# Kernel tuning notes

Measured on AMD Instinct MI355X. Metric: run time of the kernel, lower is better.

Reference implementation:

```python
import jax, jax.numpy as jnp
import numpy as np
import math

N, D, H, E = 4096, 128, 8, 131072
HD = D // H  # head_dim = 16
SCALE = 1.0 / math.sqrt(HD)


def ln(x, g, b, eps=1e-5):
    m = x.mean(-1, keepdims=True)
    v = ((x - m) ** 2).mean(-1, keepdims=True)
    return (x - m) * jax.lax.rsqrt(v + eps) * g + b


def setup_inputs() -> dict:
    key = jax.random.key(0)
    ks = iter(jax.random.split(key, 40))

    def lin(out_d, in_d):
        w = jax.random.normal(next(ks), (out_d, in_d), jnp.float32) / math.sqrt(in_d)
        b = jnp.zeros((out_d,), jnp.float32)
        return w, b

    x = jax.random.normal(next(ks), (N, D), jnp.float32)
    edge_index = jax.random.randint(next(ks), (2, E), 0, N, dtype=jnp.int64)
    wq_l, bq_l = lin(D, D); wk_l, bk_l = lin(D, D); wv_l, bv_l = lin(D, D)
    wg, bg = lin(D, 2 * D)
    wq_g, bq_g = lin(D, D); wk_g, bk_g = lin(D, D); wv_g, bv_g = lin(D, D)
    wo_g, bo_g = lin(D, D)
    wf, bf = lin(D, 2 * D)
    gf = jnp.ones((D,), jnp.float32); betaf = jnp.zeros((D,), jnp.float32)
    w1, b1 = lin(4 * D, D); w2, b2 = lin(D, 4 * D)
    g1 = jnp.ones((D,), jnp.float32); be1 = jnp.zeros((D,), jnp.float32)
    g2 = jnp.ones((D,), jnp.float32); be2 = jnp.zeros((D,), jnp.float32)
    return dict(x=x, edge_index=edge_index,
                wq_l=wq_l, bq_l=bq_l, wk_l=wk_l, bk_l=bk_l, wv_l=wv_l, bv_l=bv_l,
                wg=wg, bg=bg,
                wq_g=wq_g, bq_g=bq_g, wk_g=wk_g, bk_g=bk_g, wv_g=wv_g, bv_g=bv_g,
                wo_g=wo_g, bo_g=bo_g,
                wf=wf, bf=bf, gf=gf, betaf=betaf,
                w1=w1, b1=b1, w2=w2, b2=b2,
                g1=g1, be1=be1, g2=g2, be2=be2)


def reference(x, edge_index, wq_l, bq_l, wk_l, bk_l, wv_l, bv_l, wg, bg,
              wq_g, bq_g, wk_g, bk_g, wv_g, bv_g, wo_g, bo_g,
              wf, bf, gf, betaf, w1, b1, w2, b2, g1, be1, g2, be2):
    src, dst = edge_index[0], edge_index[1]  # PyG: j=source, i=target
    # ---- local edge-indexed multi-head attention (GraphInteractionModule) ----
    Q = (x @ wq_l.T + bq_l).reshape(N, H, HD)
    K = (x @ wk_l.T + bk_l).reshape(N, H, HD)
    V = (x @ wv_l.T + bv_l).reshape(N, H, HD)
    attn = (Q[dst] * K[src]).sum(-1) * SCALE            # [E, H]
    m = jax.ops.segment_max(attn, dst, num_segments=N)  # [N, H]
    e = jnp.exp(attn - m[dst])
    s = jax.ops.segment_sum(e, dst, num_segments=N)
    alpha = e / s[dst]                                  # segment softmax over edges into each dst
    agg = jax.ops.segment_sum(V[src] * alpha[..., None], dst, num_segments=N).reshape(N, D)
    gate = jax.nn.sigmoid(jnp.concatenate([x, agg], axis=-1) @ wg.T + bg)
    local = gate * agg + (1.0 - gate) * x
    # ---- global dense MHA over all nodes (B=1) ----
    xn = ln(x, g1, be1)
    q = (xn @ wq_g.T + bq_g).reshape(N, H, HD)
    k = (xn @ wk_g.T + bk_g).reshape(N, H, HD)
    v = (xn @ wv_g.T + bv_g).reshape(N, H, HD)
    scores = jnp.einsum('nhd,mhd->hnm', q, k) * SCALE   # [H, N, N]
    p = jax.nn.softmax(scores, axis=-1)
    go = jnp.einsum('hnm,mhd->nhd', p, v).reshape(N, D) @ wo_g.T + bo_g
    # ---- fusion + residual + FFN ----
    fused = jax.nn.relu(ln(jnp.concatenate([local, go], axis=-1) @ wf.T + bf, gf, betaf))
    h = x + fused
    h2 = ln(h, g2, be2)
    out = h + (jax.nn.gelu(h2 @ w1.T + b1, approximate=False) @ w2.T + b2)
    return out
```

## Files before the change

### kernel.cpp

```cpp
#include <hip/hip_runtime.h>
#include <math.h>

#define NN 4096
#define DM 128
#define NE 131072
#define BCAP 96
#define QSCALE 0.36067376022224085f
#define ESCALE 0.36067376022224085f

typedef short short8 __attribute__((ext_vector_type(8)));
typedef float f32x4  __attribute__((ext_vector_type(4)));
typedef unsigned int uint4v __attribute__((ext_vector_type(4)));

static __device__ __forceinline__ unsigned pk2(float lo, float hi) {
  union { float f; unsigned u; } a, b; a.f = lo; b.f = hi;
  return __builtin_amdgcn_perm(b.u + 0x8000u, a.u + 0x8000u, 0x07060302u);
}
static __device__ __forceinline__ unsigned pkp(float lo, float hi) {
  union { float f; unsigned u; } a, b; a.f = lo; b.f = hi;
  return __builtin_amdgcn_perm(b.u, a.u, 0x07060302u);
}
static __device__ __forceinline__ unsigned short f2bh(float f) {
  union { float f; unsigned u; } v; v.f = f;
  return (unsigned short)((v.u + 0x8000u) >> 16);
}
static __device__ __forceinline__ float b2f16(unsigned short u) {
  union { unsigned u; float f; } v; v.u = ((unsigned)u) << 16; return v.f;
}
static __device__ __forceinline__ float blo(unsigned u) {
  union { unsigned u; float f; } v; v.u = u << 16; return v.f;
}
static __device__ __forceinline__ float bhi(unsigned u) {
  union { unsigned u; float f; } v; v.u = u & 0xffff0000u; return v.f;
}
static __device__ __forceinline__ short8 cvt8(float4 a, float4 b) {
  uint4v u;
  u.x = pk2(a.x, a.y); u.y = pk2(a.z, a.w);
  u.z = pk2(b.x, b.y); u.w = pk2(b.z, b.w);
  return __builtin_bit_cast(short8, u);
}
static __device__ __forceinline__ int detect64(const int* __restrict__ EI) {
  int v = EI[2 * (threadIdx.x & 63) + 1];
  for (int off = 1; off < 64; off <<= 1) v |= __shfl_xor(v, off);
  return (v == 0) ? 1 : 0;
}

__global__ __launch_bounds__(256) void k_fill(float* __restrict__ out, float v, int n) {
  int i = blockIdx.x * 256 + threadIdx.x;
  if (i < n) out[i] = v;
}

#define LN1(V, GV, BV) V = (V - mean) * rstd * GV + BV
__global__ __launch_bounds__(256) void gemm_six(
    const float* __restrict__ X,
    const float* __restrict__ G1, const float* __restrict__ Be1,
    const float* __restrict__ W0, const float* __restrict__ W1, const float* __restrict__ W2,
    const float* __restrict__ W3, const float* __restrict__ W4, const float* __restrict__ W5,
    const float* __restrict__ B0, const float* __restrict__ B1, const float* __restrict__ B2,
    const float* __restrict__ B3, const float* __restrict__ B4, const float* __restrict__ B5,
    void* __restrict__ O0, void* __restrict__ O1, void* __restrict__ O2,
    void* __restrict__ O3, void* __restrict__ O4, void* __restrict__ O5,
    int* __restrict__ deg,
    const float* __restrict__ WFp, const float* __restrict__ WOg, const float* __restrict__ BOg,
    float* __restrict__ WCp, float* __restrict__ BFp)
{
  __shared__ short Asm[2][64][40];
  __shared__ short Wsm[2][64][40];
  if (blockIdx.y == 12) {
    if (blockIdx.x >= 16) return;
    const int c = threadIdx.x & 127;
    const int f0 = blockIdx.x * 8 + (threadIdx.x >> 7) * 4;
    const float* wf0 = WFp + (size_t)(f0 + 0) * 256 + 128;
    const float* wf1 = WFp + (size_t)(f0 + 1) * 256 + 128;
    const float* wf2 = WFp + (size_t)(f0 + 2) * 256 + 128;
    const float* wf3 = WFp + (size_t)(f0 + 3) * 256 + 128;
    float a0v = 0.f, a1v = 0.f, a2v = 0.f, a3v = 0.f;
    float c0 = 0.f, c1 = 0.f, c2 = 0.f, c3 = 0.f;
#pragma unroll 4
    for (int n = 0; n < 128; n++) {
      float wo = WOg[(size_t)n * 128 + c];
      float bv = BOg[n];
      float w0 = wf0[n], w1 = wf1[n], w2 = wf2[n], w3 = wf3[n];
      a0v += w0 * wo; a1v += w1 * wo; a2v += w2 * wo; a3v += w3 * wo;
      c0 += w0 * bv; c1 += w1 * bv; c2 += w2 * bv; c3 += w3 * bv;
    }
    WCp[(size_t)(f0 + 0) * 128 + c] = a0v;
    WCp[(size_t)(f0 + 1) * 128 + c] = a1v;
    WCp[(size_t)(f0 + 2) * 128 + c] = a2v;
    WCp[(size_t)(f0 + 3) * 128 + c] = a3v;
    if (c == 0) { BFp[f0] = c0; BFp[f0 + 1] = c1; BFp[f0 + 2] = c2; BFp[f0 + 3] = c3; }
    return;
  }
  if (blockIdx.x == 0 && blockIdx.y == 0) {
#pragma unroll
    for (int i = 0; i < 16; i++) deg[threadIdx.x * 16 + i] = 0;
  }
  const int g = blockIdx.y >> 1;
  const float* Wt  = (g==0)?W0:(g==1)?W1:(g==2)?W2:(g==3)?W3:(g==4)?W4:W5;
  const float* Bia = (g==0)?B0:(g==1)?B1:(g==2)?B2:(g==3)?B3:(g==4)?B4:B5;
  void* Cp         = (g==0)?O0:(g==1)?O1:(g==2)?O2:(g==3)?O3:(g==4)?O4:O5;
  const int omode  = (g==4)?3:(g==5)?2:1;
  const float osc  = (g==3)? QSCALE : (g==0)? ESCALE : 1.f;
  const int m0 = blockIdx.x * 64, n0 = (blockIdx.y & 1) * 64;
  const int tid = threadIdx.x;
  const int srow = tid >> 2, koff = (tid & 3) * 8;
  const int lane = tid & 63, wave = tid >> 6;
  const int quad = lane >> 4, m16 = lane & 15;

  const float* arow = X + (size_t)(m0 + srow) * 128 + koff;
  float4 a0[4], a1[4];
#pragma unroll
  for (int c = 0; c < 4; c++) {
    a0[c] = *(const float4*)(arow + c * 32);
    a1[c] = *(const float4*)(arow + c * 32 + 4);
  }
  if (g >= 3) {
    float s = 0.f;
#pragma unroll
    for (int c = 0; c < 4; c++)
      s += a0[c].x + a0[c].y + a0[c].z + a0[c].w + a1[c].x + a1[c].y + a1[c].z + a1[c].w;
    s += __shfl_xor(s, 1); s += __shfl_xor(s, 2);
    float mean = s * (1.0f / 128.0f);
    float v = 0.f;
#pragma unroll
    for (int c = 0; c < 4; c++) {
      float d;
      d = a0[c].x - mean; v += d*d;  d = a0[c].y - mean; v += d*d;
      d = a0[c].z - mean; v += d*d;  d = a0[c].w - mean; v += d*d;
      d = a1[c].x - mean; v += d*d;  d = a1[c].y - mean; v += d*d;
      d = a1[c].z - mean; v += d*d;  d = a1[c].w - mean; v += d*d;
    }
    v += __shfl_xor(v, 1); v += __shfl_xor(v, 2);
    float rstd = rsqrtf(v * (1.0f / 128.0f) + 1e-5f);
#pragma unroll
    for (int c = 0; c < 4; c++) {
      const int col = c * 32 + koff;
      float4 gv0 = *(const float4*)(G1 + col),  gv1 = *(const float4*)(G1 + col + 4);
      float4 bv0 = *(const float4*)(Be1 + col), bv1 = *(const float4*)(Be1 + col + 4);
      LN1(a0[c].x, gv0.x, bv0.x); LN1(a0[c].y, gv0.y, bv0.y);
      LN1(a0[c].z, gv0.z, bv0.z); LN1(a0[c].w, gv0.w, bv0.w);
      LN1(a1[c].x, gv1.x, bv1.x); LN1(a1[c].y, gv1.y, bv1.y);
      LN1(a1[c].z, gv1.z, bv1.z); LN1(a1[c].w, gv1.w, bv1.w);
    }
  }

  f32x4 acc[4];
#pragma unroll
  for (int i = 0; i < 4; i++) acc[i] = {0.f, 0.f, 0.f, 0.f};
  float4 w0r, w1r;
  {
    const float* wp = Wt + (size_t)(n0 + srow) * 128 + koff;
    w0r = *(const float4*)wp; w1r = *(const float4*)(wp + 4);
  }
#pragma unroll
  for (int c = 0; c < 4; c++) {
    const int cur = c & 1;
    *(short8*)&Asm[cur][srow][koff] = cvt8(a0[c], a1[c]);
    *(short8*)&Wsm[cur][srow][koff] = cvt8(w0r, w1r);
    __syncthreads();
    if (c < 3) {
      const float* wp = Wt + (size_t)(n0 + srow) * 128 + (c + 1) * 32 + koff;
      w0r = *(const float4*)wp; w1r = *(const float4*)(wp + 4);
    }
    short8 af = *(short8*)&Asm[cur][wave * 16 + m16][quad * 8];
#pragma unroll
    for (int nt = 0; nt < 4; nt++) {
      short8 bf = *(short8*)&Wsm[cur][nt * 16 + m16][quad * 8];
      acc[nt] = __builtin_amdgcn_mfma_f32_16x16x32_bf16(af, bf, acc[nt], 0, 0, 0);
    }
  }
#pragma unroll
  for (int nt = 0; nt < 4; nt++) {
#pragma unroll
    for (int r = 0; r < 4; r++) {
      const int m = m0 + wave * 16 + quad * 4 + r;
      const int n = n0 + nt * 16 + m16;
      float v = (acc[nt][r] + Bia[n]) * osc;
      size_t oi = (size_t)m * 128 + n;
      if (omode == 1)      ((unsigned short*)Cp)[oi] = f2bh(v);
      else if (omode == 3) ((unsigned short*)Cp)[(size_t)(n >> 4) * (NN * 16) + (size_t)m * 16 + (n & 15)] = f2bh(v);
      else                 ((unsigned short*)Cp)[(size_t)n * NN + m] = f2bh(v);
    }
  }
}

__global__ __launch_bounds__(512) void k_attn_fused(
    const unsigned short* __restrict__ Kh, const unsigned short* __restrict__ Qb,
    const unsigned short* __restrict__ VT, float* __restrict__ O,
    const int* __restrict__ EI, int* __restrict__ deg, int* __restrict__ EL)
{
  __shared__ float LO[8][4][16][16];
  __shared__ float LL[8][4][16];
  if (blockIdx.x >= 512) {
    int is64 = detect64(EI);
    int base = (blockIdx.x - 512) * 2048 + threadIdx.x;
#pragma unroll
    for (int r = 0; r < 4; r++) {
      int e = base + r * 512;
      int d = is64 ? EI[2*(NE+e)] : EI[NE+e];
      d = min(max(d, 0), NN-1);
      int slot = atomicAdd(&deg[d], 1);
      if (slot < BCAP) EL[d * BCAP + slot] = e;
    }
    return;
  }
  const int h = blockIdx.x >> 6, qt = blockIdx.x & 63;
  const int tid = threadIdx.x, lane = tid & 63, wave = tid >> 6;
  const int quad = lane >> 4, m16 = lane & 15;
  const int r0 = qt * 64;
  const short8 z8 = {0,0,0,0,0,0,0,0};
  const f32x4  z4 = {0.f,0.f,0.f,0.f};
  short8 qf[4] = {z8, z8, z8, z8};
  if (quad < 2) {
#pragma unroll
    for (int j = 0; j < 4; j++)
      qf[j] = *(const short8*)(Qb + (size_t)(r0 + j * 16 + m16) * DM + h * 16 + quad * 8);
  }
  short8 ones;
#pragma unroll
  for (int i = 0; i < 8; i++) ones[i] = (short)0x3F80;
  const int kperm = (m16 >> 2) * 8 + (m16 & 3);
  const int kbase = wave * 512;
  const unsigned short* khead = Kh + (size_t)h * (NN * 16);
  f32x4 acc[4] = {z4, z4, z4, z4};
  f32x4 acc2[4] = {z4, z4, z4, z4};
  short8 a0 = z8, a1 = z8, a2 = z8, a3 = z8;
  for (int kt = 0; kt < 8; kt++) {
    const int key0 = kbase + kt * 64;
    if (quad < 2) {
      const unsigned short* kp = khead + (size_t)(key0 + kperm) * 16 + quad * 8;
      a0 = *(const short8*)kp;
      a1 = *(const short8*)(kp + 4 * 16);
      a2 = *(const short8*)(kp + 32 * 16);
      a3 = *(const short8*)(kp + 36 * 16);
    }
    const unsigned short* vp = VT + (size_t)(h * 16 + m16) * NN + key0 + quad * 8;
    short8 av0 = *(const short8*)vp;
    short8 av1 = *(const short8*)(vp + 32);
#pragma unroll
    for (int j = 0; j < 4; j++) {
      f32x4 s0 = __builtin_amdgcn_mfma_f32_16x16x32_bf16(a0, qf[j], z4, 0, 0, 0);
      f32x4 s1 = __builtin_amdgcn_mfma_f32_16x16x32_bf16(a1, qf[j], z4, 0, 0, 0);
      f32x4 s2 = __builtin_amdgcn_mfma_f32_16x16x32_bf16(a2, qf[j], z4, 0, 0, 0);
      f32x4 s3 = __builtin_amdgcn_mfma_f32_16x16x32_bf16(a3, qf[j], z4, 0, 0, 0);
      float e0 = __builtin_amdgcn_exp2f(s0[0]), e1 = __builtin_amdgcn_exp2f(s0[1]);
      float e2 = __builtin_amdgcn_exp2f(s0[2]), e3 = __builtin_amdgcn_exp2f(s0[3]);
      float e4 = __builtin_amdgcn_exp2f(s1[0]), e5 = __builtin_amdgcn_exp2f(s1[1]);
      float e6 = __builtin_amdgcn_exp2f(s1[2]), e7 = __builtin_amdgcn_exp2f(s1[3]);
      uint4v u;
      u.x = pkp(e0, e1); u.y = pkp(e2, e3); u.z = pkp(e4, e5); u.w = pkp(e6, e7);
      short8 p0 = __builtin_bit_cast(short8, u);
      float f0 = __builtin_amdgcn_exp2f(s2[0]), f1 = __builtin_amdgcn_exp2f(s2[1]);
      float f2 = __builtin_amdgcn_exp2f(s2[2]), f3 = __builtin_amdgcn_exp2f(s2[3]);
      float f4 = __builtin_amdgcn_exp2f(s3[0]), f5 = __builtin_amdgcn_exp2f(s3[1]);
      float f6 = __builtin_amdgcn_exp2f(s3[2]), f7 = __builtin_amdgcn_exp2f(s3[3]);
      uint4v w;
      w.x = pkp(f0, f1); w.y = pkp(f2, f3); w.z = pkp(f4, f5); w.w = pkp(f6, f7);
      short8 p1 = __builtin_bit_cast(short8, w);
      acc[j]  = __builtin_amdgcn_mfma_f32_16x16x32_bf16(av0, p0, acc[j], 0, 0, 0);
      acc[j]  = __builtin_amdgcn_mfma_f32_16x16x32_bf16(av1, p1, acc[j], 0, 0, 0);
      acc2[j] = __builtin_amdgcn_mfma_f32_16x16x32_bf16(ones, p0, acc2[j], 0, 0, 0);
      acc2[j] = __builtin_amdgcn_mfma_f32_16x16x32_bf16(ones, p1, acc2[j], 0, 0, 0);
    }
  }
#pragma unroll
  for (int j = 0; j < 4; j++) {
    float4 a4; a4.x = acc[j][0]; a4.y = acc[j][1]; a4.z = acc[j][2]; a4.w = acc[j][3];
    *(float4*)&LO[wave][j][m16][quad * 4] = a4;
    if (lane < 16) LL[wave][j][lane] = acc2[j][0];
  }
  __syncthreads();
  if (wave < 4) {
    const int j = wave;
    float4 o = *(float4*)&LO[0][j][m16][quad * 4];
    float lt = LL[0][j][m16];
#pragma unroll
    for (int w2 = 1; w2 < 8; w2++) {
      float4 t = *(float4*)&LO[w2][j][m16][quad * 4];
      o.x += t.x; o.y += t.y; o.z += t.z; o.w += t.w;
      lt += LL[w2][j][m16];
    }
    float inv = 1.0f / fmaxf(lt, 1e-30f);
    float4 r4; r4.x = o.x * inv; r4.y = o.y * inv; r4.z = o.z * inv; r4.w = o.w * inv;
    *(float4*)(O + (size_t)(r0 + j * 16 + m16) * DM + h * 16 + quad * 4) = r4;
  }
}

__global__ __launch_bounds__(256) void k_edge_agg3(const int* __restrict__ EI,
    const int* __restrict__ deg, const int* __restrict__ elist,
    const unsigned short* __restrict__ Vl, const unsigned short* __restrict__ Kb,
    const unsigned short* __restrict__ Qb, float* __restrict__ AG) {
  __shared__ float PS[2][128];
  __shared__ float SSH[2][2][8];
  __shared__ float SC[2][BCAP][8];
  int is64 = detect64(EI);
  int tid = threadIdx.x;
  int dsti = tid >> 7;
  int half = (tid >> 6) & 1;
  int lane = tid & 63;
  int d = blockIdx.x * 2 + dsti;
  int degd = min(deg[d], BCAP), start = d * BCAP;
  int hh = lane >> 3;
  unsigned qv = *(const unsigned*)(Qb + (size_t)d * DM + 2 * lane);
  float q0 = blo(qv), q1 = bhi(qv);
  float ss = 0.f;
  int i = half;
  for (; i + 6 < degd; i += 8) {
    int e0 = elist[start+i], e1 = elist[start+i+2], e2 = elist[start+i+4], e3 = elist[start+i+6];
    e0 = min(max(e0,0),NE-1); e1 = min(max(e1,0),NE-1);
    e2 = min(max(e2,0),NE-1); e3 = min(max(e3,0),NE-1);
    int s0 = is64 ? EI[2*e0] : EI[e0];
    int s1 = is64 ? EI[2*e1] : EI[e1];
    int s2 = is64 ? EI[2*e2] : EI[e2];
    int s3 = is64 ? EI[2*e3] : EI[e3];
    s0 = min(max(s0,0),NN-1); s1 = min(max(s1,0),NN-1);
    s2 = min(max(s2,0),NN-1); s3 = min(max(s3,0),NN-1);
    unsigned k0 = *(const unsigned*)(Kb + (size_t)s0 * DM + 2 * lane);
    unsigned k1 = *(const unsigned*)(Kb + (size_t)s1 * DM + 2 * lane);
    unsigned k2 = *(const unsigned*)(Kb + (size_t)s2 * DM + 2 * lane);
    unsigned k3 = *(const unsigned*)(Kb + (size_t)s3 * DM + 2 * lane);
    float p0 = q0 * blo(k0) + q1 * bhi(k0);
    float p1 = q0 * blo(k1) + q1 * bhi(k1);
    float p2 = q0 * blo(k2) + q1 * bhi(k2);
    float p3 = q0 * blo(k3) + q1 * bhi(k3);
    p0 += __shfl_xor(p0,1); p0 += __shfl_xor(p0,2); p0 += __shfl_xor(p0,4);
    p1 += __shfl_xor(p1,1); p1 += __shfl_xor(p1,2); p1 += __shfl_xor(p1,4);
    p2 += __shfl_xor(p2,1); p2 += __shfl_xor(p2,2); p2 += __shfl_xor(p2,4);
    p3 += __shfl_xor(p3,1); p3 += __shfl_xor(p3,2); p3 += __shfl_xor(p3,4);
    float ev0 = __builtin_amdgcn_exp2f(fminf(p0, 43.0f));
    float ev1 = __builtin_amdgcn_exp2f(fminf(p1, 43.0f));
    float ev2 = __builtin_amdgcn_exp2f(fminf(p2, 43.0f));
    float ev3 = __builtin_amdgcn_exp2f(fminf(p3, 43.0f));
    if ((lane & 7) == 0) {
      SC[dsti][i][hh] = ev0;   SC[dsti][i+2][hh] = ev1;
      SC[dsti][i+4][hh] = ev2; SC[dsti][i+6][hh] = ev3;
    }
    ss += ev0 + ev1 + ev2 + ev3;
  }
  for (; i < degd; i += 2) {
    int e = elist[start + i];
    e = min(max(e,0),NE-1);
    int s = is64 ? EI[2*e] : EI[e];
    s = min(max(s, 0), NN-1);
    unsigned k = *(const unsigned*)(Kb + (size_t)s * DM + 2 * lane);
    float p = q0 * blo(k) + q1 * bhi(k);
    p += __shfl_xor(p,1); p += __shfl_xor(p,2); p += __shfl_xor(p,4);
    float ev = __builtin_amdgcn_exp2f(fminf(p, 43.0f));
    if ((lane & 7) == 0) SC[dsti][i][hh] = ev;
    ss += ev;
  }
  if ((lane & 7) == 0) SSH[dsti][half][hh] = ss;
  __syncthreads();
  float inv = 1.0f / fmaxf(SSH[dsti][0][hh] + SSH[dsti][1][hh], 1e-30f);
  float ax = 0.f, ay = 0.f;
  i = half;
  for (; i + 6 < degd; i += 8) {
    int e0 = elist[start+i], e1 = elist[start+i+2], e2 = elist[start+i+4], e3 = elist[start+i+6];
    e0 = min(max(e0,0),NE-1); e1 = min(max(e1,0),NE-1);
    e2 = min(max(e2,0),NE-1); e3 = min(max(e3,0),NE-1);
    int s0 = is64 ? EI[2*e0] : EI[e0];
    int s1 = is64 ? EI[2*e1] : EI[e1];
    int s2 = is64 ? EI[2*e2] : EI[e2];
    int s3 = is64 ? EI[2*e3] : EI[e3];
    s0 = min(max(s0,0),NN-1); s1 = min(max(s1,0),NN-1);
    s2 = min(max(s2,0),NN-1); s3 = min(max(s3,0),NN-1);
    float w0 = SC[dsti][i][hh] * inv;
    float w1 = SC[dsti][i+2][hh] * inv;
    float w2 = SC[dsti][i+4][hh] * inv;
    float w3 = SC[dsti][i+6][hh] * inv;
    unsigned v0 = *(const unsigned*)(Vl + (size_t)s0 * DM + 2 * lane);
    unsigned v1 = *(const unsigned*)(Vl + (size_t)s1 * DM + 2 * lane);
    unsigned v2 = *(const unsigned*)(Vl + (size_t)s2 * DM + 2 * lane);
    unsigned v3 = *(const unsigned*)(Vl + (size_t)s3 * DM + 2 * lane);
    ax += w0 * blo(v0) + w1 * blo(v1) + w2 * blo(v2) + w3 * blo(v3);
    ay += w0 * bhi(v0) + w1 * bhi(v1) + w2 * bhi(v2) + w3 * bhi(v3);
  }
  for (; i < degd; i += 2) {
    int e = elist[start + i];
    e = min(max(e,0),NE-1);
    int s = is64 ? EI[2*e] : EI[e];
    s = min(max(s, 0), NN-1);
    float a = SC[dsti][i][hh] * inv;
    unsigned v = *(const unsigned*)(Vl + (size_t)s * DM + 2 * lane);
    ax += a * blo(v);
    ay += a * bhi(v);
  }
  if (half == 1) { PS[dsti][2*lane] = ax; PS[dsti][2*lane+1] = ay; }
  __syncthreads();
  if (half == 0) {
    float2 r; r.x = ax + PS[dsti][2*lane]; r.y = ay + PS[dsti][2*lane+1];
    *(float2*)(AG + (size_t)d * DM + 2 * lane) = r;
  }
}

__global__ __launch_bounds__(256) void gemm_gatefuse(
    const float* __restrict__ X, const float* __restrict__ AGG, const float* __restrict__ GO,
    const float* __restrict__ Wg, const float* __restrict__ Bg,
    const float* __restrict__ WF, const float* __restrict__ WC,
    const float* __restrict__ BF, const float* __restrict__ BFOLD,
    float* __restrict__ TMPF)
{
  __shared__ short Asm[64][40];
  __shared__ short Wsm[128][40];
  __shared__ short Lsm[4][64][40];
  const int m0 = blockIdx.x * 64, n0 = blockIdx.y * 64;
  const int tid = threadIdx.x;
  const int srow = tid >> 2, koff = (tid & 3) * 8;
  const int wrow = tid >> 1, koff2 = (tid & 1) * 16;
  const int lane = tid & 63, wave = tid >> 6;
  const int quad = lane >> 4, m16 = lane & 15;

  f32x4 acc8[8];
#pragma unroll
  for (int i = 0; i < 8; i++) acc8[i] = {0.f, 0.f, 0.f, 0.f};
  for (int k0 = 0; k0 < 256; k0 += 32) {
    const int kg = k0 + koff;
    const float* ap = (kg < 128) ? (X + (size_t)(m0 + srow) * 128 + kg)
                                 : (AGG + (size_t)(m0 + srow) * 128 + (kg - 128));
    float4 a0 = *(const float4*)ap, a1 = *(const float4*)(ap + 4);
    const float* wp = Wg + (size_t)wrow * 256 + k0 + koff2;
    float4 w0 = *(const float4*)wp,       w1v = *(const float4*)(wp + 4);
    float4 w2v = *(const float4*)(wp + 8), w3v = *(const float4*)(wp + 12);
    __syncthreads();
    *(short8*)&Asm[srow][koff] = cvt8(a0, a1);
    *(short8*)&Wsm[wrow][koff2]     = cvt8(w0, w1v);
    *(short8*)&Wsm[wrow][koff2 + 8] = cvt8(w2v, w3v);
    __syncthreads();
    short8 af = *(short8*)&Asm[wave * 16 + m16][quad * 8];
#pragma unroll
    for (int nt = 0; nt < 8; nt++) {
      short8 bf = *(short8*)&Wsm[nt * 16 + m16][quad * 8];
      acc8[nt] = __builtin_amdgcn_mfma_f32_16x16x32_bf16(af, bf, acc8[nt], 0, 0, 0);
    }
  }
  __syncthreads();
#pragma unroll
  for (int nt = 0; nt < 8; nt++) {
#pragma unroll
    for (int r = 0; r < 4; r++) {
      const int mr = wave * 16 + quad * 4 + r;
      const int n = nt * 16 + m16;
      float v = acc8[nt][r] + Bg[n];
      size_t oi = (size_t)(m0 + mr) * 128 + n;
      float gg = 1.0f / (1.0f + __expf(fminf(fmaxf(-v, -80.f), 80.f)));
      float loc = gg * AGG[oi] + (1.0f - gg) * X[oi];
      Lsm[n >> 5][mr][n & 31] = (short)f2bh(loc);
    }
  }

  f32x4 acc[4];
#pragma unroll
  for (int i = 0; i < 4; i++) acc[i] = {0.f, 0.f, 0.f, 0.f};
  for (int k0 = 0; k0 < 256; k0 += 32) {
    const int c = k0 >> 5;
    float4 a0g, a1g;
    if (c >= 4) {
      const float* ap = GO + (size_t)(m0 + srow) * 128 + (k0 - 128) + koff;
      a0g = *(const float4*)ap; a1g = *(const float4*)(ap + 4);
    }
    const float* wp = (c < 4) ? (WF + (size_t)(n0 + srow) * 256 + k0 + koff)
                              : (WC + (size_t)(n0 + srow) * 128 + (k0 - 128) + koff);
    float4 w0 = *(const float4*)wp, w1v = *(const float4*)(wp + 4);
    __syncthreads();
    if (c >= 4) *(short8*)&Asm[srow][koff] = cvt8(a0g, a1g);
    *(short8*)&Wsm[srow][koff] = cvt8(w0, w1v);
    __syncthreads();
    short8 af = (c < 4) ? *(short8*)&Lsm[c][wave * 16 + m16][quad * 8]
                        : *(short8*)&Asm[wave * 16 + m16][quad * 8];
#pragma unroll
    for (int nt = 0; nt < 4; nt++) {
      short8 bf = *(short8*)&Wsm[nt * 16 + m16][quad * 8];
      acc[nt] = __builtin_amdgcn_mfma_f32_16x16x32_bf16(af, bf, acc[nt], 0, 0, 0);
    }
  }
#pragma unroll
  for (int nt = 0; nt < 4; nt++) {
#pragma unroll
    for (int r = 0; r < 4; r++) {
      const int m = m0 + wave * 16 + quad * 4 + r;
      const int n = n0 + nt * 16 + m16;
      TMPF[(size_t)m * 128 + n] = acc[nt][r] + BF[n] + BFOLD[n];
    }
  }
}

__global__ __launch_bounds__(256) void gemm_ffn1(
    const float* __restrict__ T, const float* __restrict__ X,
    const float* __restrict__ Gf, const float* __restrict__ Bef,
    const float* __restrict__ G2, const float* __restrict__ Be2,
    const float* __restrict__ W1, const float* __restrict__ B1,
    float* __restrict__ H, unsigned short* __restrict__ T1)
{
  __shared__ short Asm[2][64][40];
  __shared__ short Wsm[2][64][40];
  const int m0 = blockIdx.x * 64, n0 = blockIdx.y * 64;
  const int tid = threadIdx.x;
  const int srow = tid >> 2, koff = (tid & 3) * 8;
  const int lane = tid & 63, wave = tid >> 6;
  const int quad = lane >> 4, m16 = lane & 15;

  const float* trow = T + (size_t)(m0 + srow) * 128 + koff;
  const float* xrow = X + (size_t)(m0 + srow) * 128 + koff;
  float4 a0[4], a1[4];
#pragma unroll
  for (int c = 0; c < 4; c++) {
    a0[c] = *(const float4*)(trow + c * 32);
    a1[c] = *(const float4*)(trow + c * 32 + 4);
  }
  {
    float s = 0.f;
#pragma unroll
    for (int c = 0; c < 4; c++)
      s += a0[c].x + a0[c].y + a0[c].z + a0[c].w + a1[c].x + a1[c].y + a1[c].z + a1[c].w;
    s += __shfl_xor(s, 1); s += __shfl_xor(s, 2);
    float mean = s * (1.0f / 128.0f);
    float v = 0.f;
#pragma unroll
    for (int c = 0; c < 4; c++) {
      float d;
      d = a0[c].x - mean; v += d*d;  d = a0[c].y - mean; v += d*d;
      d = a0[c].z - mean; v += d*d;  d = a0[c].w - mean; v += d*d;
      d = a1[c].x - mean; v += d*d;  d = a1[c].y - mean; v += d*d;
      d = a1[c].z - mean; v += d*d;  d = a1[c].w - mean; v += d*d;
    }
    v += __shfl_xor(v, 1); v += __shfl_xor(v, 2);
    float rstd = rsqrtf(v * (1.0f / 128.0f) + 1e-5f);
#pragma unroll
    for (int c = 0; c < 4; c++) {
      const int col = c * 32 + koff;
      float4 gv0 = *(const float4*)(Gf + col),  gv1 = *(const float4*)(Gf + col + 4);
      float4 bv0 = *(const float4*)(Bef + col), bv1 = *(const float4*)(Bef + col + 4);
      float4 x0 = *(const float4*)(xrow + c * 32), x1 = *(const float4*)(xrow + c * 32 + 4);
      LN1(a0[c].x, gv0.x, bv0.x); LN1(a0[c].y, gv0.y, bv0.y);
      LN1(a0[c].z, gv0.z, bv0.z); LN1(a0[c].w, gv0.w, bv0.w);
      LN1(a1[c].x, gv1.x, bv1.x); LN1(a1[c].y, gv1.y, bv1.y);
      LN1(a1[c].z, gv1.z, bv1.z); LN1(a1[c].w, gv1.w, bv1.w);
      a0[c].x = x0.x + fmaxf(a0[c].x, 0.f); a0[c].y = x0.y + fmaxf(a0[c].y, 0.f);
      a0[c].z = x0.z + fmaxf(a0[c].z, 0.f); a0[c].w = x0.w + fmaxf(a0[c].w, 0.f);
      a1[c].x = x1.x + fmaxf(a1[c].x, 0.f); a1[c].y = x1.y + fmaxf(a1[c].y, 0.f);
      a1[c].z = x1.z + fmaxf(a1[c].z, 0.f); a1[c].w = x1.w + fmaxf(a1[c].w, 0.f);
      if (blockIdx.y == 0) {
        *(float4*)(H + (size_t)(m0 + srow) * 128 + c * 32 + koff)     = a0[c];
        *(float4*)(H + (size_t)(m0 + srow) * 128 + c * 32 + koff + 4) = a1[c];
      }
    }
  }
  {
    float s = 0.f;
#pragma unroll
    for (int c = 0; c < 4; c++)
      s += a0[c].x + a0[c].y + a0[c].z + a0[c].w + a1[c].x + a1[c].y + a1[c].z + a1[c].w;
    s += __shfl_xor(s, 1); s += __shfl_xor(s, 2);
    float mean = s * (1.0f / 128.0f);
    float v = 0.f;
#pragma unroll
    for (int c = 0; c < 4; c++) {
      float d;
      d = a0[c].x - mean; v += d*d;  d = a0[c].y - mean; v += d*d;
      d = a0[c].z - mean; v += d*d;  d = a0[c].w - mean; v += d*d;
      d = a1[c].x - mean; v += d*d;  d = a1[c].y - mean; v += d*d;
      d = a1[c].z - mean; v += d*d;  d = a1[c].w - mean; v += d*d;
    }
    v += __shfl_xor(v, 1); v += __shfl_xor(v, 2);
    float rstd = rsqrtf(v * (1.0f / 128.0f) + 1e-5f);
#pragma unroll
    for (int c = 0; c < 4; c++) {
      const int col = c * 32 + koff;
      float4 gv0 = *(const float4*)(G2 + col),  gv1 = *(const float4*)(G2 + col + 4);
      float4 bv0 = *(const float4*)(Be2 + col), bv1 = *(const float4*)(Be2 + col + 4);
      LN1(a0[c].x, gv0.x, bv0.x); LN1(a0[c].y, gv0.y, bv0.y);
      LN1(a0[c].z, gv0.z, bv0.z); LN1(a0[c].w, gv0.w, bv0.w);
      LN1(a1[c].x, gv1.x, bv1.x); LN1(a1[c].y, gv1.y, bv1.y);
      LN1(a1[c].z, gv1.z, bv1.z); LN1(a1[c].w, gv1.w, bv1.w);
    }
  }

  f32x4 acc[4];
#pragma unroll
  for (int i = 0; i < 4; i++) acc[i] = {0.f, 0.f, 0.f, 0.f};
  float4 w0r, w1r;
  {
    const float* wp = W1 + (size_t)(n0 + srow) * 128 + koff;
    w0r = *(const float4*)wp; w1r = *(const float4*)(wp + 4);
  }
#pragma unroll
  for (int c = 0; c < 4; c++) {
    const int cur = c & 1;
    *(short8*)&Asm[cur][srow][koff] = cvt8(a0[c], a1[c]);
    *(short8*)&Wsm[cur][srow][koff] = cvt8(w0r, w1r);
    __syncthreads();
    if (c < 3) {
      const float* wp = W1 + (size_t)(n0 + srow) * 128 + (c + 1) * 32 + koff;
      w0r = *(const float4*)wp; w1r = *(const float4*)(wp + 4);
    }
    short8 af = *(short8*)&Asm[cur][wave * 16 + m16][quad * 8];
#pragma unroll
    for (int nt = 0; nt < 4; nt++) {
      short8 bf = *(short8*)&Wsm[cur][nt * 16 + m16][quad * 8];
      acc[nt] = __builtin_amdgcn_mfma_f32_16x16x32_bf16(af, bf, acc[nt], 0, 0, 0);
    }
  }
#pragma unroll
  for (int nt = 0; nt < 4; nt++) {
#pragma unroll
    for (int r = 0; r < 4; r++) {
      const int m = m0 + wave * 16 + quad * 4 + r;
      const int n = n0 + nt * 16 + m16;
      float v = acc[nt][r] + B1[n];
      v = 0.5f * v * (1.0f + erff(v * 0.70710678118654752f));
      T1[(size_t)m * 512 + n] = f2bh(v);
    }
  }
}

__global__ __launch_bounds__(256) void gemm_w2b(
    const unsigned short* __restrict__ A,
    const float* __restrict__ Wt, const float* __restrict__ Bias,
    const float* __restrict__ Res, float* __restrict__ Cp)
{
  __shared__ short Asm[2][64][40];
  __shared__ short Wsm[2][64][40];
  const int m0 = blockIdx.x * 64, n0 = blockIdx.y * 64;
  const int tid = threadIdx.x;
  const int srow = tid >> 2, koff = (tid & 3) * 8;
  const int lane = tid & 63, wave = tid >> 6;
  const int quad = lane >> 4, m16 = lane & 15;
  f32x4 acc[4];
#pragma unroll
  for (int i = 0; i < 4; i++) acc[i] = {0.f, 0.f, 0.f, 0.f};

  short8 avr; float4 w0r, w1r;
  {
    avr = *(const short8*)(A + (size_t)(m0 + srow) * 512 + koff);
    const float* wp = Wt + (size_t)(n0 + srow) * 512 + koff;
    w0r = *(const float4*)wp; w1r = *(const float4*)(wp + 4);
  }
  for (int k0 = 0; k0 < 512; k0 += 32) {
    const int cur = (k0 >> 5) & 1;
    *(short8*)&Asm[cur][srow][koff] = avr;
    *(short8*)&Wsm[cur][srow][koff] = cvt8(w0r, w1r);
    __syncthreads();
    if (k0 + 32 < 512) {
      const int kg = k0 + 32 + koff;
      avr = *(const short8*)(A + (size_t)(m0 + srow) * 512 + kg);
      const float* wp = Wt + (size_t)(n0 + srow) * 512 + kg;
      w0r = *(const float4*)wp; w1r = *(const float4*)(wp + 4);
    }
    short8 af = *(short8*)&Asm[cur][wave * 16 + m16][quad * 8];
#pragma unroll
    for (int nt = 0; nt < 4; nt++) {
      short8 bf = *(short8*)&Wsm[cur][nt * 16 + m16][quad * 8];
      acc[nt] = __builtin_amdgcn_mfma_f32_16x16x32_bf16(af, bf, acc[nt], 0, 0, 0);
    }
  }
#pragma unroll
  for (int nt = 0; nt < 4; nt++) {
#pragma unroll
    for (int r = 0; r < 4; r++) {
      const int m = m0 + wave * 16 + quad * 4 + r;
      const int n = n0 + nt * 16 + m16;
      size_t oi = (size_t)m * 128 + n;
      Cp[oi] = acc[nt][r] + Bias[n] + Res[oi];
    }
  }
}

extern "C" void kernel_launch(void* const* d_in, const int* in_sizes, int n_in,
                              void* d_out, int out_size, void* d_ws, size_t ws_size,
                              hipStream_t stream) {
  const float* x     = (const float*)d_in[0];
  const int*   ei    = (const int*)  d_in[1];
  const float* wq_l  = (const float*)d_in[2];  const float* bq_l = (const float*)d_in[3];
  const float* wk_l  = (const float*)d_in[4];  const float* bk_l = (const float*)d_in[5];
  const float* wv_l  = (const float*)d_in[6];  const float* bv_l = (const float*)d_in[7];
  const float* wg    = (const float*)d_in[8];  const float* bg   = (const float*)d_in[9];
  const float* wq_g  = (const float*)d_in[10]; const float* bq_g = (const float*)d_in[11];
  const float* wk_g  = (const float*)d_in[12]; const float* bk_g = (const float*)d_in[13];
  const float* wv_g  = (const float*)d_in[14]; const float* bv_g = (const float*)d_in[15];
  const float* wo_g  = (const float*)d_in[16]; const float* bo_g = (const float*)d_in[17];
  const float* wf    = (const float*)d_in[18]; const float* bff  = (const float*)d_in[19];
  const float* gf    = (const float*)d_in[20]; const float* betaf= (const float*)d_in[21];
  const float* w1    = (const float*)d_in[22]; const float* b1   = (const float*)d_in[23];
  const float* w2    = (const float*)d_in[24]; const float* b2   = (const float*)d_in[25];
  const float* g1    = (const float*)d_in[26]; const float* be1  = (const float*)d_in[27];
  const float* g2    = (const float*)d_in[28]; const float* be2  = (const float*)d_in[29];
  float* out = (float*)d_out;

  const size_t NEED = (size_t)4223104 * 4;
  if (ws_size < NEED) {
    k_fill<<<2048, 256, 0, stream>>>(out, 100.0f, NN*DM);
    return;
  }

  float* W = (float*)d_ws;
  unsigned short* lQb   = (unsigned short*)(W + 0);
  unsigned short* lKb   = (unsigned short*)(W + 524288);
  unsigned short* lV    = (unsigned short*)(W + 1048576);
  float*          go    = W + 1835008;
  unsigned short* qgb   = (unsigned short*)(W + 2359296);
  unsigned short* kgb   = (unsigned short*)(W + 2621440);
  unsigned short* vgT   = (unsigned short*)(W + 2883584);
  float*          tmpf  = W + 1310720;
  float*          h     = W + 2621440;
  unsigned short* t1    = (unsigned short*)(W + 0);
  int* deg    = (int*)(W + 3145728);
  float* Wc    = W + 3289088;
  float* bfold = W + 3305472;
  int* elist96 = (int*)(W + 3305600);
  float*          agg   = W + 3698816;

  dim3 b256(256);

  gemm_six<<<dim3(64,13), b256, 0, stream>>>(x, g1, be1,
      wq_l, wk_l, wv_l, wq_g, wk_g, wv_g,
      bq_l, bk_l, bv_l, bq_g, bk_g, bv_g,
      lQb, lKb, lV, qgb, kgb, vgT, deg,
      wf, wo_g, bo_g, Wc, bfold);

  k_attn_fused<<<576, dim3(512), 0, stream>>>(kgb, qgb, vgT, go, ei, deg, elist96);

  k_edge_agg3<<<2048, b256, 0, stream>>>(ei, deg, elist96, lV, lKb, lQb, agg);

  gemm_gatefuse<<<dim3(64,2), b256, 0, stream>>>(x, agg, go, wg, bg, wf, Wc, bff, bfold, tmpf);
  gemm_ffn1<<<dim3(64,8), b256, 0, stream>>>(tmpf, x, gf, betaf, g2, be2, w1, b1, h, t1);
  gemm_w2b<<<dim3(64,2), b256, 0, stream>>>(t1, w2, b2, h, out);
}
```

Baseline: 207.7 us.

## Fuse edge aggregation into attention kernel and move edge bucketing into projection GEMM

Edge bucketing by destination (the atomicAdd into deg and the edge-list writes) moves from the attention kernel into extra blocks of the projection GEMM kernel. The deg array is now zeroed with hipMemsetAsync before that kernel instead of inside it. The local edge softmax and aggregation, previously a separate kernel, now run as extra blocks of the dense attention kernel, with shared memory unioned between the two roles. The aim is to drop one launch and let the sparse gather work overlap with the dense attention blocks, at the cost of an extra memset operation and a larger, mixed-role grid.

```diff
diff --git a/kernel.cpp b/kernel.cpp
--- a/kernel.cpp
+++ b/kernel.cpp
@@ -62,10 +62,24 @@
     void* __restrict__ O3, void* __restrict__ O4, void* __restrict__ O5,
     int* __restrict__ deg,
     const float* __restrict__ WFp, const float* __restrict__ WOg, const float* __restrict__ BOg,
-    float* __restrict__ WCp, float* __restrict__ BFp)
+    float* __restrict__ WCp, float* __restrict__ BFp,
+    const int* __restrict__ EI, int* __restrict__ EL)
 {
   __shared__ short Asm[2][64][40];
   __shared__ short Wsm[2][64][40];
+  if (blockIdx.y == 13) {
+    int is64 = detect64(EI);
+    int base = blockIdx.x * 2048 + threadIdx.x;
+#pragma unroll
+    for (int r = 0; r < 8; r++) {
+      int e = base + r * 256;
+      int d = is64 ? EI[2*(NE+e)] : EI[NE+e];
+      d = min(max(d, 0), NN-1);
+      int slot = atomicAdd(&deg[d], 1);
+      if (slot < BCAP) EL[d * BCAP + slot] = e;
+    }
+    return;
+  }
   if (blockIdx.y == 12) {
     if (blockIdx.x >= 16) return;
     const int c = threadIdx.x & 127;
@@ -91,10 +105,6 @@
     if (c == 0) { BFp[f0] = c0; BFp[f0 + 1] = c1; BFp[f0 + 2] = c2; BFp[f0 + 3] = c3; }
     return;
   }
-  if (blockIdx.x == 0 && blockIdx.y == 0) {
-#pragma unroll
-    for (int i = 0; i < 16; i++) deg[threadIdx.x * 16 + i] = 0;
-  }
   const int g = blockIdx.y >> 1;
   const float* Wt  = (g==0)?W0:(g==1)?W1:(g==2)?W2:(g==3)?W3:(g==4)?W4:W5;
   const float* Bia = (g==0)?B0:(g==1)?B1:(g==2)?B2:(g==3)?B3:(g==4)?B4:B5;
@@ -184,23 +194,115 @@
   }
 }
 
-__global__ __launch_bounds__(512) void k_attn_fused(
+__global__ __launch_bounds__(512) void k_attn_agg(
     const unsigned short* __restrict__ Kh, const unsigned short* __restrict__ Qb,
     const unsigned short* __restrict__ VT, float* __restrict__ O,
-    const int* __restrict__ EI, int* __restrict__ deg, int* __restrict__ EL)
+    const int* __restrict__ EI, const int* __restrict__ deg, const int* __restrict__ elist,
+    const unsigned short* __restrict__ Vl, const unsigned short* __restrict__ Kb,
+    const unsigned short* __restrict__ Qb16, float* __restrict__ AG)
 {
-  __shared__ float LO[8][4][16][16];
-  __shared__ float LL[8][4][16];
+  __shared__ union {
+    struct { float LO[8][4][16][16]; float LL[8][4][16]; } a;
+    struct { float PS[4][128]; float SSH[4][2][8]; float SC[4][BCAP][8]; } g;
+  } S;
   if (blockIdx.x >= 512) {
     int is64 = detect64(EI);
-    int base = (blockIdx.x - 512) * 2048 + threadIdx.x;
-#pragma unroll
-    for (int r = 0; r < 4; r++) {
-      int e = base + r * 512;
-      int d = is64 ? EI[2*(NE+e)] : EI[NE+e];
-      d = min(max(d, 0), NN-1);
-      int slot = atomicAdd(&deg[d], 1);
-      if (slot < BCAP) EL[d * BCAP + slot] = e;
+    int tid = threadIdx.x;
+    int dsti = tid >> 7;
+    int half = (tid >> 6) & 1;
+    int lane = tid & 63;
+    int d = (blockIdx.x - 512) * 4 + dsti;
+    int degd = min(deg[d], BCAP), start = d * BCAP;
+    int hh = lane >> 3;
+    unsigned qv = *(const unsigned*)(Qb16 + (size_t)d * DM + 2 * lane);
+    float q0 = blo(qv), q1 = bhi(qv);
+    float ss = 0.f;
+    int i = half;
+    for (; i + 6 < degd; i += 8) {
+      int e0 = elist[start+i], e1 = elist[start+i+2], e2 = elist[start+i+4], e3 = elist[start+i+6];
+      e0 = min(max(e0,0),NE-1); e1 = min(max(e1,0),NE-1);
+      e2 = min(max(e2,0),NE-1); e3 = min(max(e3,0),NE-1);
+      int s0 = is64 ? EI[2*e0] : EI[e0];
+      int s1 = is64 ? EI[2*e1] : EI[e1];
+      int s2 = is64 ? EI[2*e2] : EI[e2];
+      int s3 = is64 ? EI[2*e3] : EI[e3];
+      s0 = min(max(s0,0),NN-1); s1 = min(max(s1,0),NN-1);
+      s2 = min(max(s2,0),NN-1); s3 = min(max(s3,0),NN-1);
+      unsigned k0 = *(const unsigned*)(Kb + (size_t)s0 * DM + 2 * lane);
+      unsigned k1 = *(const unsigned*)(Kb + (size_t)s1 * DM + 2 * lane);
+      unsigned k2 = *(const unsigned*)(Kb + (size_t)s2 * DM + 2 * lane);
+      unsigned k3 = *(const unsigned*)(Kb + (size_t)s3 * DM + 2 * lane);
+      float p0 = q0 * blo(k0) + q1 * bhi(k0);
+      float p1 = q0 * blo(k1) + q1 * bhi(k1);
+      float p2 = q0 * blo(k2) + q1 * bhi(k2);
+      float p3 = q0 * blo(k3) + q1 * bhi(k3);
+      p0 += __shfl_xor(p0,1); p0 += __shfl_xor(p0,2); p0 += __shfl_xor(p0,4);
+      p1 += __shfl_xor(p1,1); p1 += __shfl_xor(p1,2); p1 += __shfl_xor(p1,4);
+      p2 += __shfl_xor(p2,1); p2 += __shfl_xor(p2,2); p2 += __shfl_xor(p2,4);
+      p3 += __shfl_xor(p3,1); p3 += __shfl_xor(p3,2); p3 += __shfl_xor(p3,4);
+      float ev0 = __builtin_amdgcn_exp2f(fminf(p0, 43.0f));
+      float ev1 = __builtin_amdgcn_exp2f(fminf(p1, 43.0f));
+      float ev2 = __builtin_amdgcn_exp2f(fminf(p2, 43.0f));
+      float ev3 = __builtin_amdgcn_exp2f(fminf(p3, 43.0f));
+      if ((lane & 7) == 0) {
+        S.g.SC[dsti][i][hh] = ev0;   S.g.SC[dsti][i+2][hh] = ev1;
+        S.g.SC[dsti][i+4][hh] = ev2; S.g.SC[dsti][i+6][hh] = ev3;
+      }
+      ss += ev0 + ev1 + ev2 + ev3;
+    }
+    for (; i < degd; i += 2) {
+      int e = elist[start + i];
+      e = min(max(e,0),NE-1);
+      int s = is64 ? EI[2*e] : EI[e];
+      s = min(max(s, 0), NN-1);
+      unsigned k = *(const unsigned*)(Kb + (size_t)s * DM + 2 * lane);
+      float p = q0 * blo(k) + q1 * bhi(k);
+      p += __shfl_xor(p,1); p += __shfl_xor(p,2); p += __shfl_xor(p,4);
+      float ev = __builtin_amdgcn_exp2f(fminf(p, 43.0f));
+      if ((lane & 7) == 0) S.g.SC[dsti][i][hh] = ev;
+      ss += ev;
+    }
+    if ((lane & 7) == 0) S.g.SSH[dsti][half][hh] = ss;
+    __syncthreads();
+    float inv = 1.0f / fmaxf(S.g.SSH[dsti][0][hh] + S.g.SSH[dsti][1][hh], 1e-30f);
+    float ax = 0.f, ay = 0.f;
+    i = half;
+    for (; i + 6 < degd; i += 8) {
+      int e0 = elist[start+i], e1 = elist[start+i+2], e2 = elist[start+i+4], e3 = elist[start+i+6];
+      e0 = min(max(e0,0),NE-1); e1 = min(max(e1,0),NE-1);
+      e2 = min(max(e2,0),NE-1); e3 = min(max(e3,0),NE-1);
+      int s0 = is64 ? EI[2*e0] : EI[e0];
+      int s1 = is64 ? EI[2*e1] : EI[e1];
+      int s2 = is64 ? EI[2*e2] : EI[e2];
+      int s3 = is64 ? EI[2*e3] : EI[e3];
+      s0 = min(max(s0,0),NN-1); s1 = min(max(s1,0),NN-1);
+      s2 = min(max(s2,0),NN-1); s3 = min(max(s3,0),NN-1);
+      float w0 = S.g.SC[dsti][i][hh] * inv;
+      float w1 = S.g.SC[dsti][i+2][hh] * inv;
+      float w2 = S.g.SC[dsti][i+4][hh] * inv;
+      float w3 = S.g.SC[dsti][i+6][hh] * inv;
+      unsigned v0 = *(const unsigned*)(Vl + (size_t)s0 * DM + 2 * lane);
+      unsigned v1 = *(const unsigned*)(Vl + (size_t)s1 * DM + 2 * lane);
+      unsigned v2 = *(const unsigned*)(Vl + (size_t)s2 * DM + 2 * lane);
+      unsigned v3 = *(const unsigned*)(Vl + (size_t)s3 * DM + 2 * lane);
+      ax += w0 * blo(v0) + w1 * blo(v1) + w2 * blo(v2) + w3 * blo(v3);
+      ay += w0 * bhi(v0) + w1 * bhi(v1) + w2 * bhi(v2) + w3 * bhi(v3);
+    }
+    for (; i < degd; i += 2) {
+      int e = elist[start + i];
+      e = min(max(e,0),NE-1);
+      int s = is64 ? EI[2*e] : EI[e];
+      s = min(max(s, 0), NN-1);
+      float a = S.g.SC[dsti][i][hh] * inv;
+      unsigned v = *(const unsigned*)(Vl + (size_t)s * DM + 2 * lane);
+      ax += a * blo(v);
+      ay += a * bhi(v);
+    }
+    if (half == 1) { S.g.PS[dsti][2*lane] = ax; S.g.PS[dsti][2*lane+1] = ay; }
+    __syncthreads();
+    if (half == 0) {
+      float2 r; r.x = ax + S.g.PS[dsti][2*lane]; r.y = ay + S.g.PS[dsti][2*lane+1];
+      *(float2*)(AG + (size_t)d * DM + 2 * lane) = r;
     }
     return;
   }
@@ -266,130 +368,23 @@
 #pragma unroll
   for (int j = 0; j < 4; j++) {
     float4 a4; a4.x = acc[j][0]; a4.y = acc[j][1]; a4.z = acc[j][2]; a4.w = acc[j][3];
-    *(float4*)&LO[wave][j][m16][quad * 4] = a4;
-    if (lane < 16) LL[wave][j][lane] = acc2[j][0];
+    *(float4*)&S.a.LO[wave][j][m16][quad * 4] = a4;
+    if (lane < 16) S.a.LL[wave][j][lane] = acc2[j][0];
   }
   __syncthreads();
   if (wave < 4) {
     const int j = wave;
-    float4 o = *(float4*)&LO[0][j][m16][quad * 4];
-    float lt = LL[0][j][m16];
+    float4 o = *(float4*)&S.a.LO[0][j][m16][quad * 4];
+    float lt = S.a.LL[0][j][m16];
 #pragma unroll
     for (int w2 = 1; w2 < 8; w2++) {
-      float4 t = *(float4*)&LO[w2][j][m16][quad * 4];
+      float4 t = *(float4*)&S.a.LO[w2][j][m16][quad * 4];
       o.x += t.x; o.y += t.y; o.z += t.z; o.w += t.w;
-      lt += LL[w2][j][m16];
+      lt += S.a.LL[w2][j][m16];
     }
     float inv = 1.0f / fmaxf(lt, 1e-30f);
     float4 r4; r4.x = o.x * inv; r4.y = o.y * inv; r4.z = o.z * inv; r4.w = o.w * inv;
     *(float4*)(O + (size_t)(r0 + j * 16 + m16) * DM + h * 16 + quad * 4) = r4;
-  }
-}
-
-__global__ __launch_bounds__(256) void k_edge_agg3(const int* __restrict__ EI,
-    const int* __restrict__ deg, const int* __restrict__ elist,
-    const unsigned short* __restrict__ Vl, const unsigned short* __restrict__ Kb,
-    const unsigned short* __restrict__ Qb, float* __restrict__ AG) {
-  __shared__ float PS[2][128];
-  __shared__ float SSH[2][2][8];
-  __shared__ float SC[2][BCAP][8];
-  int is64 = detect64(EI);
-  int tid = threadIdx.x;
-  int dsti = tid >> 7;
-  int half = (tid >> 6) & 1;
-  int lane = tid & 63;
-  int d = blockIdx.x * 2 + dsti;
-  int degd = min(deg[d], BCAP), start = d * BCAP;
-  int hh = lane >> 3;
-  unsigned qv = *(const unsigned*)(Qb + (size_t)d * DM + 2 * lane);
-  float q0 = blo(qv), q1 = bhi(qv);
-  float ss = 0.f;
-  int i = half;
-  for (; i + 6 < degd; i += 8) {
-    int e0 = elist[start+i], e1 = elist[start+i+2], e2 = elist[start+i+4], e3 = elist[start+i+6];
-    e0 = min(max(e0,0),NE-1); e1 = min(max(e1,0),NE-1);
-    e2 = min(max(e2,0),NE-1); e3 = min(max(e3,0),NE-1);
-    int s0 = is64 ? EI[2*e0] : EI[e0];
-    int s1 = is64 ? EI[2*e1] : EI[e1];
-    int s2 = is64 ? EI[2*e2] : EI[e2];
-    int s3 = is64 ? EI[2*e3] : EI[e3];
-    s0 = min(max(s0,0),NN-1); s1 = min(max(s1,0),NN-1);
-    s2 = min(max(s2,0),NN-1); s3 = min(max(s3,0),NN-1);
-    unsigned k0 = *(const unsigned*)(Kb + (size_t)s0 * DM + 2 * lane);
-    unsigned k1 = *(const unsigned*)(Kb + (size_t)s1 * DM + 2 * lane);
-    unsigned k2 = *(const unsigned*)(Kb + (size_t)s2 * DM + 2 * lane);
-    unsigned k3 = *(const unsigned*)(Kb + (size_t)s3 * DM + 2 * lane);
-    float p0 = q0 * blo(k0) + q1 * bhi(k0);
-    float p1 = q0 * blo(k1) + q1 * bhi(k1);
-    float p2 = q0 * blo(k2) + q1 * bhi(k2);
-    float p3 = q0 * blo(k3) + q1 * bhi(k3);
-    p0 += __shfl_xor(p0,1); p0 += __shfl_xor(p0,2); p0 += __shfl_xor(p0,4);
-    p1 += __shfl_xor(p1,1); p1 += __shfl_xor(p1,2); p1 += __shfl_xor(p1,4);
-    p2 += __shfl_xor(p2,1); p2 += __shfl_xor(p2,2); p2 += __shfl_xor(p2,4);
-    p3 += __shfl_xor(p3,1); p3 += __shfl_xor(p3,2); p3 += __shfl_xor(p3,4);
-    float ev0 = __builtin_amdgcn_exp2f(fminf(p0, 43.0f));
-    float ev1 = __builtin_amdgcn_exp2f(fminf(p1, 43.0f));
-    float ev2 = __builtin_amdgcn_exp2f(fminf(p2, 43.0f));
-    float ev3 = __builtin_amdgcn_exp2f(fminf(p3, 43.0f));
-    if ((lane & 7) == 0) {
-      SC[dsti][i][hh] = ev0;   SC[dsti][i+2][hh] = ev1;
-      SC[dsti][i+4][hh] = ev2; SC[dsti][i+6][hh] = ev3;
-    }
-    ss += ev0 + ev1 + ev2 + ev3;
-  }
-  for (; i < degd; i += 2) {
-    int e = elist[start + i];
-    e = min(max(e,0),NE-1);
-    int s = is64 ? EI[2*e] : EI[e];
-    s = min(max(s, 0), NN-1);
-    unsigned k = *(const unsigned*)(Kb + (size_t)s * DM + 2 * lane);
-    float p = q0 * blo(k) + q1 * bhi(k);
-    p += __shfl_xor(p,1); p += __shfl_xor(p,2); p += __shfl_xor(p,4);
-    float ev = __builtin_amdgcn_exp2f(fminf(p, 43.0f));
-    if ((lane & 7) == 0) SC[dsti][i][hh] = ev;
-    ss += ev;
-  }
-  if ((lane & 7) == 0) SSH[dsti][half][hh] = ss;
-  __syncthreads();
-  float inv = 1.0f / fmaxf(SSH[dsti][0][hh] + SSH[dsti][1][hh], 1e-30f);
-  float ax = 0.f, ay = 0.f;
-  i = half;
-  for (; i + 6 < degd; i += 8) {
-    int e0 = elist[start+i], e1 = elist[start+i+2], e2 = elist[start+i+4], e3 = elist[start+i+6];
-    e0 = min(max(e0,0),NE-1); e1 = min(max(e1,0),NE-1);
-    e2 = min(max(e2,0),NE-1); e3 = min(max(e3,0),NE-1);
-    int s0 = is64 ? EI[2*e0] : EI[e0];
-    int s1 = is64 ? EI[2*e1] : EI[e1];
-    int s2 = is64 ? EI[2*e2] : EI[e2];
-    int s3 = is64 ? EI[2*e3] : EI[e3];
-    s0 = min(max(s0,0),NN-1); s1 = min(max(s1,0),NN-1);
-    s2 = min(max(s2,0),NN-1); s3 = min(max(s3,0),NN-1);
-    float w0 = SC[dsti][i][hh] * inv;
-    float w1 = SC[dsti][i+2][hh] * inv;
-    float w2 = SC[dsti][i+4][hh] * inv;
-    float w3 = SC[dsti][i+6][hh] * inv;
-    unsigned v0 = *(const unsigned*)(Vl + (size_t)s0 * DM + 2 * lane);
-    unsigned v1 = *(const unsigned*)(Vl + (size_t)s1 * DM + 2 * lane);
-    unsigned v2 = *(const unsigned*)(Vl + (size_t)s2 * DM + 2 * lane);
-    unsigned v3 = *(const unsigned*)(Vl + (size_t)s3 * DM + 2 * lane);
-    ax += w0 * blo(v0) + w1 * blo(v1) + w2 * blo(v2) + w3 * blo(v3);
-    ay += w0 * bhi(v0) + w1 * bhi(v1) + w2 * bhi(v2) + w3 * bhi(v3);
-  }
-  for (; i < degd; i += 2) {
-    int e = elist[start + i];
-    e = min(max(e,0),NE-1);
-    int s = is64 ? EI[2*e] : EI[e];
-    s = min(max(s, 0), NN-1);
-    float a = SC[dsti][i][hh] * inv;
-    unsigned v = *(const unsigned*)(Vl + (size_t)s * DM + 2 * lane);
-    ax += a * blo(v);
-    ay += a * bhi(v);
-  }
-  if (half == 1) { PS[dsti][2*lane] = ax; PS[dsti][2*lane+1] = ay; }
-  __syncthreads();
-  if (half == 0) {
-    float2 r; r.x = ax + PS[dsti][2*lane]; r.y = ay + PS[dsti][2*lane+1];
-    *(float2*)(AG + (size_t)d * DM + 2 * lane) = r;
   }
 }
 
@@ -419,11 +414,11 @@
                                  : (AGG + (size_t)(m0 + srow) * 128 + (kg - 128));
     float4 a0 = *(const float4*)ap, a1 = *(const float4*)(ap + 4);
     const float* wp = Wg + (size_t)wrow * 256 + k0 + koff2;
-    float4 w0 = *(const float4*)wp,       w1v = *(const float4*)(wp + 4);
+    float4 w0 = *(const float4*)wp,       float4w1 = *(const float4*)(wp + 4);
     float4 w2v = *(const float4*)(wp + 8), w3v = *(const float4*)(wp + 12);
     __syncthreads();
     *(short8*)&Asm[srow][koff] = cvt8(a0, a1);
-    *(short8*)&Wsm[wrow][koff2]     = cvt8(w0, w1v);
+    *(short8*)&Wsm[wrow][koff2]     = cvt8(w0, float4w1);
     *(short8*)&Wsm[wrow][koff2 + 8] = cvt8(w2v, w3v);
     __syncthreads();
     short8 af = *(short8*)&Asm[wave * 16 + m16][quad * 8];
@@ -711,15 +706,16 @@
 
   dim3 b256(256);
 
-  gemm_six<<<dim3(64,13), b256, 0, stream>>>(x, g1, be1,
+  hipMemsetAsync(deg, 0, NN * sizeof(int), stream);
+
+  gemm_six<<<dim3(64,14), b256, 0, stream>>>(x, g1, be1,
       wq_l, wk_l, wv_l, wq_g, wk_g, wv_g,
       bq_l, bk_l, bv_l, bq_g, bk_g, bv_g,
       lQb, lKb, lV, qgb, kgb, vgT, deg,
-      wf, wo_g, bo_g, Wc, bfold);
-
-  k_attn_fused<<<576, dim3(512), 0, stream>>>(kgb, qgb, vgT, go, ei, deg, elist96);
-
-  k_edge_agg3<<<2048, b256, 0, stream>>>(ei, deg, elist96, lV, lKb, lQb, agg);
+      wf, wo_g, bo_g, Wc, bfold, ei, elist96);
+
+  k_attn_agg<<<1536, dim3(512), 0, stream>>>(kgb, qgb, vgT, go, ei, deg, elist96,
+                                             lV, lKb, lQb, agg);
 
   gemm_gatefuse<<<dim3(64,2), b256, 0, stream>>>(x, agg, go, wg, bg, wf, Wc, bff, bfold, tmpf);
   gemm_ffn1<<<dim3(64,8), b256, 0, stream>>>(tmpf, x, gf, betaf, g2, be2, w1, b1, h, t1);
```

Result: no change. 210.5 us (+1.4%).
